# Kernel optimization log

Hardware: AMD Instinct MI355X
Metric: run time of the kernel (lower is better)

## Reference

```python
import jax, jax.numpy as jnp
import numpy as np

INPUT_SIZE = 1024
HIDDEN_SIZE = 1024
BATCH = 8192


def setup_inputs() -> dict:
    key = jax.random.key(0)
    ks = jax.random.split(key, 10)
    s_in = 1.0 / np.sqrt(INPUT_SIZE)
    s_h = 1.0 / np.sqrt(HIDDEN_SIZE)
    return {
        "input": jax.random.normal(ks[0], (BATCH, INPUT_SIZE), jnp.float32),
        "hx": jax.random.normal(ks[1], (BATCH, HIDDEN_SIZE), jnp.float32),
        # weights stored [in, out] (transpose of torch Linear)
        "W_ih": jax.random.uniform(ks[2], (INPUT_SIZE, 2 * HIDDEN_SIZE), jnp.float32, -s_in, s_in),
        "b_ih": jax.random.uniform(ks[3], (2 * HIDDEN_SIZE,), jnp.float32, -s_in, s_in),
        "W_hh": jax.random.uniform(ks[4], (HIDDEN_SIZE, 2 * HIDDEN_SIZE), jnp.float32, -s_h, s_h),
        "b_hh": jax.random.uniform(ks[5], (2 * HIDDEN_SIZE,), jnp.float32, -s_h, s_h),
        "W_c": jax.random.uniform(ks[6], (INPUT_SIZE, HIDDEN_SIZE), jnp.float32, -s_in, s_in),
        "b_c": jax.random.uniform(ks[7], (HIDDEN_SIZE,), jnp.float32, -s_in, s_in),
        "W_hc": jax.random.uniform(ks[8], (HIDDEN_SIZE, HIDDEN_SIZE), jnp.float32, -s_h, s_h),
        "b_hc": jax.random.uniform(ks[9], (HIDDEN_SIZE,), jnp.float32, -s_h, s_h),
    }


def reference(input, hx, W_ih, b_ih, W_hh, b_hh, W_c, b_c, W_hc, b_hc):
    H = hx.shape[1]
    gates = jax.nn.sigmoid(input @ W_ih + b_ih + hx @ W_hh + b_hh)  # [B, 2H]
    z_t, r_t = gates[:, :H], gates[:, H:]
    candidate = jnp.tanh(input @ W_c + b_c + r_t * (hx @ W_hc + b_hc))
    return (1.0 - z_t) * hx + z_t * candidate
```

## Files before the change

kernel.cpp:

```cpp
#include <hip/hip_runtime.h>
#include <hip/hip_bf16.h>
#include <cmath>


typedef __attribute__((ext_vector_type(8))) short bf16x8;
typedef __attribute__((ext_vector_type(4))) float f32x4;
typedef unsigned int u32;

typedef const __attribute__((address_space(1))) u32 gu32;
typedef __attribute__((address_space(3))) u32 su32;

__device__ __forceinline__ unsigned short f2bf(float f) {
  union { float f; u32 u; } v; v.f = f;
  u32 u = v.u;
  u += 0x7FFFu + ((u >> 16) & 1u);
  return (unsigned short)(u >> 16);
}
__device__ __forceinline__ void gload16(void* ldsp, const void* gp) {
  __builtin_amdgcn_global_load_lds((gu32*)gp, (su32*)ldsp, 16, 0, 0);
}
__device__ __forceinline__ float sigmf(float x) { return 1.0f / (1.0f + __expf(-x)); }

__global__ __launch_bounds__(256) void cvt_all(
    const float* __restrict__ In, const float* __restrict__ Hx,
    const float* __restrict__ Wih, const float* __restrict__ Whh,
    const float* __restrict__ Wc,  const float* __restrict__ Whc,
    unsigned short* __restrict__ wsIn, unsigned short* __restrict__ wsHx,
    unsigned short* __restrict__ wsWih, unsigned short* __restrict__ wsWhh,
    unsigned short* __restrict__ wsWc,  unsigned short* __restrict__ wsWhc)
{
  int bid = blockIdx.x;
  if (bid < 8192) {
    int gid = bid * 256 + threadIdx.x;
    const float* src; unsigned short* dst; int idx;
    if (gid < (1 << 20)) { src = In; dst = wsIn; idx = gid; }
    else                 { src = Hx; dst = wsHx; idx = gid - (1 << 20); }
    int m = idx >> 7, t = idx & 127;
    const float4* s = (const float4*)(src + (size_t)m * 1024 + t * 8);
    float4 a = s[0], b = s[1];
    int row = m & 127;
    size_t tile = (size_t)(m >> 7) * 32 + (t >> 2);
    int sw = (t & 3) ^ ((row >> 1) & 3);
    bf16x8 v;
    v[0] = (short)f2bf(a.x); v[1] = (short)f2bf(a.y); v[2] = (short)f2bf(a.z); v[3] = (short)f2bf(a.w);
    v[4] = (short)f2bf(b.x); v[5] = (short)f2bf(b.y); v[6] = (short)f2bf(b.z); v[7] = (short)f2bf(b.w);
    *(bf16x8*)(dst + tile * 4096 + row * 32 + sw * 8) = v;
  } else {
    int wb = bid - 8192;
    const float* W; unsigned short* dst; int NW; int local;
    if (wb < 1024)      { W = Wih; dst = wsWih; NW = 2048; local = wb; }
    else if (wb < 2048) { W = Whh; dst = wsWhh; NW = 2048; local = wb - 1024; }
    else if (wb < 2560) { W = Wc;  dst = wsWc;  NW = 1024; local = wb - 2048; }
    else                { W = Whc; dst = wsWhc; NW = 1024; local = wb - 2560; }
    int nb = local >> 5, kb = local & 31;
    int n  = nb * 64 + (threadIdx.x & 63);
    int k0 = kb * 32 + (threadIdx.x >> 6) * 8;
    bf16x8 v;
    #pragma unroll
    for (int b = 0; b < 8; ++b) v[b] = (short)f2bf(W[(size_t)(k0 + b) * NW + n]);
    int row = n & 63;
    size_t tile = (size_t)(n >> 6) * 32 + (k0 >> 5);
    int sw = ((k0 >> 3) & 3) ^ ((row >> 1) & 3);
    *(bf16x8*)(dst + tile * 2048 + row * 32 + sw * 8) = v;
  }
}

__global__ __launch_bounds__(256, 2) void gru_gemm(
    const unsigned short* __restrict__ wsIn, const unsigned short* __restrict__ wsHx,
    const unsigned short* __restrict__ wsWih, const unsigned short* __restrict__ wsWhh,
    const unsigned short* __restrict__ wsWc, const unsigned short* __restrict__ wsWhc,
    const float* __restrict__ Hx,
    const float* __restrict__ bih, const float* __restrict__ bhh,
    const float* __restrict__ bc, const float* __restrict__ bhc,
    float* __restrict__ out)
{
  __shared__ unsigned short lds[40960];
  const int tid  = threadIdx.x;
  const int lane = tid & 63;
  const int wave = tid >> 6;
  const int wm = wave >> 1, wn = wave & 1;
  const int bid = blockIdx.x;
  const int swz = (bid & 7) * 128 + (bid >> 3);
  const int j = swz & 15;
  const int i = swz >> 4;

  const unsigned short* srcB[10];
  int strd[10];
  #pragma unroll
  for (int c0 = 0; c0 < 10; ++c0) {
    int c = wave * 10 + c0;
    const unsigned short* p; int st;
    if (c < 8)       { p = wsIn + (size_t)i * 131072 + c * 512;        st = 4096; }
    else if (c < 16) { p = wsHx + (size_t)i * 131072 + (c - 8) * 512;  st = 4096; }
    else {
      int t = (c - 16) >> 2, cc = (c - 16) & 3;
      const unsigned short* base; int nb;
      if (t == 0)      { base = wsWih; nb = j; }
      else if (t == 1) { base = wsWih; nb = j + 16; }
      else if (t == 2) { base = wsWhh; nb = j; }
      else if (t == 3) { base = wsWhh; nb = j + 16; }
      else if (t == 4) { base = wsWc;  nb = j; }
      else             { base = wsWhc; nb = j; }
      p = base + (size_t)nb * 65536 + cc * 512;
      st = 2048;
    }
    srcB[c0] = p + lane * 8;
    strd[c0] = st;
  }
  const int stageOff = (wave * 10) * 512;

  f32x4 accZ[4][2], accR[4][2], accC[4][2], accH[4][2];
  #pragma unroll
  for (int a = 0; a < 4; ++a)
    #pragma unroll
    for (int b = 0; b < 2; ++b) {
      accZ[a][b] = (f32x4)(0.0f); accR[a][b] = (f32x4)(0.0f);
      accC[a][b] = (f32x4)(0.0f); accH[a][b] = (f32x4)(0.0f);
    }

  const int r15 = lane & 15;
  const int q   = lane >> 4;

  int aOff[4], wOff[2];
  #pragma unroll
  for (int mr = 0; mr < 4; ++mr) {
    int row = wm * 64 + mr * 16 + r15;
    aOff[mr] = row * 32 + ((q ^ ((row >> 1) & 3)) << 3);
  }
  #pragma unroll
  for (int nr = 0; nr < 2; ++nr) {
    int row = wn * 32 + nr * 16 + r15;
    wOff[nr] = row * 32 + ((q ^ ((row >> 1) & 3)) << 3);
  }

  auto stage = [&](int bufBase, int s) {
    #pragma unroll
    for (int c0 = 0; c0 < 10; ++c0)
      gload16((void*)&lds[bufBase + stageOff + c0 * 512],
              (const void*)(srcB[c0] + (size_t)s * strd[c0]));
  };

  auto compute = [&](const unsigned short* __restrict__ L) {
    bf16x8 aIn[4], aHx[4];
    #pragma unroll
    for (int mr = 0; mr < 4; ++mr) {
      aIn[mr] = *(const bf16x8*)&L[aOff[mr]];
      aHx[mr] = *(const bf16x8*)&L[4096 + aOff[mr]];
    }
    bf16x8 wf[6][2];
    #pragma unroll
    for (int t = 0; t < 6; ++t)
      #pragma unroll
      for (int nr = 0; nr < 2; ++nr)
        wf[t][nr] = *(const bf16x8*)&L[8192 + t * 2048 + wOff[nr]];

    #pragma unroll
    for (int mr = 0; mr < 4; ++mr)
      #pragma unroll
      for (int nr = 0; nr < 2; ++nr) {
        accZ[mr][nr] = __builtin_amdgcn_mfma_f32_16x16x32_bf16(aIn[mr], wf[0][nr], accZ[mr][nr], 0, 0, 0);
        accZ[mr][nr] = __builtin_amdgcn_mfma_f32_16x16x32_bf16(aHx[mr], wf[2][nr], accZ[mr][nr], 0, 0, 0);
        accR[mr][nr] = __builtin_amdgcn_mfma_f32_16x16x32_bf16(aIn[mr], wf[1][nr], accR[mr][nr], 0, 0, 0);
        accR[mr][nr] = __builtin_amdgcn_mfma_f32_16x16x32_bf16(aHx[mr], wf[3][nr], accR[mr][nr], 0, 0, 0);
        accC[mr][nr] = __builtin_amdgcn_mfma_f32_16x16x32_bf16(aIn[mr], wf[4][nr], accC[mr][nr], 0, 0, 0);
        accH[mr][nr] = __builtin_amdgcn_mfma_f32_16x16x32_bf16(aHx[mr], wf[5][nr], accH[mr][nr], 0, 0, 0);
      }
  };

  stage(0, 0);
  __syncthreads();

  #pragma unroll 1
  for (int it = 0; it < 16; ++it) {
    const int s = it * 2;
    stage(20480, s + 1);
    compute(&lds[0]);
    __syncthreads();
    if (it < 15) stage(0, s + 2);
    compute(&lds[20480]);
    __syncthreads();
  }

  const int n0 = j * 64 + wn * 32;
  const int m0 = i * 128 + wm * 64;
  #pragma unroll
  for (int nr = 0; nr < 2; ++nr) {
    int n = n0 + nr * 16 + r15;
    float bz  = bih[n] + bhh[n];
    float br  = bih[1024 + n] + bhh[1024 + n];
    float bcv = bc[n], bhcv = bhc[n];
    #pragma unroll
    for (int mr = 0; mr < 4; ++mr) {
      #pragma unroll
      for (int v = 0; v < 4; ++v) {
        int m = m0 + mr * 16 + q * 4 + v;
        float z  = sigmf(accZ[mr][nr][v] + bz);
        float rr = sigmf(accR[mr][nr][v] + br);
        float cd = tanhf(accC[mr][nr][v] + bcv + rr * (accH[mr][nr][v] + bhcv));
        float h  = Hx[(size_t)m * 1024 + n];
        out[(size_t)m * 1024 + n] = (1.0f - z) * h + z * cd;
      }
    }
  }
}

__global__ __launch_bounds__(256) void gru_fallback(
    const float* __restrict__ In, const float* __restrict__ Hx,
    const float* __restrict__ Wih, const float* __restrict__ bih,
    const float* __restrict__ Whh, const float* __restrict__ bhh,
    const float* __restrict__ Wc, const float* __restrict__ bc,
    const float* __restrict__ Whc, const float* __restrict__ bhc,
    float* __restrict__ out)
{
  __shared__ float sIn[64][17], sHx[64][17];
  __shared__ float sW[6][16][68];
  const int tid = threadIdx.x;
  const int j = blockIdx.x & 15, i = blockIdx.x >> 4;
  const int tx = tid & 15, ty = tid >> 4;
  float accZ[4][4] = {}, accR[4][4] = {}, accC[4][4] = {}, accH[4][4] = {};
  const int ms = tid >> 2, kq = (tid & 3) * 4;
  const int wk = tid >> 4, wn4 = (tid & 15) * 4;
  for (int k0 = 0; k0 < 1024; k0 += 16) {
    __syncthreads();
    {
      float4 a = *(const float4*)&In[(size_t)(i * 64 + ms) * 1024 + k0 + kq];
      sIn[ms][kq] = a.x; sIn[ms][kq + 1] = a.y; sIn[ms][kq + 2] = a.z; sIn[ms][kq + 3] = a.w;
      float4 b = *(const float4*)&Hx[(size_t)(i * 64 + ms) * 1024 + k0 + kq];
      sHx[ms][kq] = b.x; sHx[ms][kq + 1] = b.y; sHx[ms][kq + 2] = b.z; sHx[ms][kq + 3] = b.w;
    }
    {
      float4 w0 = *(const float4*)&Wih[(size_t)(k0 + wk) * 2048 + j * 64 + wn4];
      float4 w1 = *(const float4*)&Wih[(size_t)(k0 + wk) * 2048 + 1024 + j * 64 + wn4];
      float4 w2 = *(const float4*)&Whh[(size_t)(k0 + wk) * 2048 + j * 64 + wn4];
      float4 w3 = *(const float4*)&Whh[(size_t)(k0 + wk) * 2048 + 1024 + j * 64 + wn4];
      float4 w4 = *(const float4*)&Wc[(size_t)(k0 + wk) * 1024 + j * 64 + wn4];
      float4 w5 = *(const float4*)&Whc[(size_t)(k0 + wk) * 1024 + j * 64 + wn4];
      sW[0][wk][wn4] = w0.x; sW[0][wk][wn4+1] = w0.y; sW[0][wk][wn4+2] = w0.z; sW[0][wk][wn4+3] = w0.w;
      sW[1][wk][wn4] = w1.x; sW[1][wk][wn4+1] = w1.y; sW[1][wk][wn4+2] = w1.z; sW[1][wk][wn4+3] = w1.w;
      sW[2][wk][wn4] = w2.x; sW[2][wk][wn4+1] = w2.y; sW[2][wk][wn4+2] = w2.z; sW[2][wk][wn4+3] = w2.w;
      sW[3][wk][wn4] = w3.x; sW[3][wk][wn4+1] = w3.y; sW[3][wk][wn4+2] = w3.z; sW[3][wk][wn4+3] = w3.w;
      sW[4][wk][wn4] = w4.x; sW[4][wk][wn4+1] = w4.y; sW[4][wk][wn4+2] = w4.z; sW[4][wk][wn4+3] = w4.w;
      sW[5][wk][wn4] = w5.x; sW[5][wk][wn4+1] = w5.y; sW[5][wk][wn4+2] = w5.z; sW[5][wk][wn4+3] = w5.w;
    }
    __syncthreads();
    for (int kk = 0; kk < 16; ++kk) {
      float aI[4], aH[4];
      #pragma unroll
      for (int im = 0; im < 4; ++im) { aI[im] = sIn[ty * 4 + im][kk]; aH[im] = sHx[ty * 4 + im][kk]; }
      #pragma unroll
      for (int jn = 0; jn < 4; ++jn) {
        float w0 = sW[0][kk][tx * 4 + jn], w1 = sW[1][kk][tx * 4 + jn], w2 = sW[2][kk][tx * 4 + jn];
        float w3 = sW[3][kk][tx * 4 + jn], w4 = sW[4][kk][tx * 4 + jn], w5 = sW[5][kk][tx * 4 + jn];
        #pragma unroll
        for (int im = 0; im < 4; ++im) {
          accZ[im][jn] += aI[im] * w0 + aH[im] * w2;
          accR[im][jn] += aI[im] * w1 + aH[im] * w3;
          accC[im][jn] += aI[im] * w4;
          accH[im][jn] += aH[im] * w5;
        }
      }
    }
  }
  #pragma unroll
  for (int jn = 0; jn < 4; ++jn) {
    int n = j * 64 + tx * 4 + jn;
    float bz  = bih[n] + bhh[n];
    float br  = bih[1024 + n] + bhh[1024 + n];
    float bcv = bc[n], bhcv = bhc[n];
    #pragma unroll
    for (int im = 0; im < 4; ++im) {
      int m = i * 64 + ty * 4 + im;
      float z  = sigmf(accZ[im][jn] + bz);
      float rr = sigmf(accR[im][jn] + br);
      float cd = tanhf(accC[im][jn] + bcv + rr * (accH[im][jn] + bhcv));
      float h  = Hx[(size_t)m * 1024 + n];
      out[(size_t)m * 1024 + n] = (1.0f - z) * h + z * cd;
    }
  }
}

extern "C" void kernel_launch(void* const* d_in, const int* in_sizes, int n_in,
                              void* d_out, int out_size, void* d_ws, size_t ws_size,
                              hipStream_t stream) {
  const float* In  = (const float*)d_in[0];
  const float* Hx  = (const float*)d_in[1];
  const float* Wih = (const float*)d_in[2];
  const float* bih = (const float*)d_in[3];
  const float* Whh = (const float*)d_in[4];
  const float* bhh = (const float*)d_in[5];
  const float* Wc  = (const float*)d_in[6];
  const float* bc  = (const float*)d_in[7];
  const float* Whc = (const float*)d_in[8];
  const float* bhc = (const float*)d_in[9];
  float* out = (float*)d_out;

  const size_t WS_NEED = 46137344ull;
  if (ws_size >= WS_NEED) {
    unsigned short* ws    = (unsigned short*)d_ws;
    unsigned short* wsIn  = ws;
    unsigned short* wsHx  = ws + 8388608;
    unsigned short* wsWih = ws + 16777216;
    unsigned short* wsWhh = ws + 18874368;
    unsigned short* wsWc  = ws + 20971520;
    unsigned short* wsWhc = ws + 22020096;
    cvt_all<<<11264, 256, 0, stream>>>(In, Hx, Wih, Whh, Wc, Whc,
                                       wsIn, wsHx, wsWih, wsWhh, wsWc, wsWhc);
    gru_gemm<<<1024, 256, 0, stream>>>(wsIn, wsHx, wsWih, wsWhh, wsWc, wsWhc,
                                       Hx, bih, bhh, bc, bhc, out);
  } else {
    gru_fallback<<<2048, 256, 0, stream>>>(In, Hx, Wih, bih, Whh, bhh, Wc, bc, Whc, bhc, out);
  }
}
```

Before: 139.3 us.

## Load weight fragments directly from global memory, stage only activations in LDS

The GEMM kernel now stages only the input and hidden-state tiles through LDS. Each wave reads its weight fragments straight from the pre-swizzled workspace in global memory into registers, which shrinks shared memory from 80KB to 32KB per block. Block indexing also changes from the grouped swizzle to i = bid & 63, j = bid >> 6, so consecutive blocks share the same weight tile. The aim is to cut LDS traffic and footprint and raise occupancy. The cost is uncoalesced-ish global/L2 weight reads on the critical path, since each wave loads its own weights with no cross-wave reuse through LDS.

```diff
diff --git a/kernel.cpp b/kernel.cpp
--- a/kernel.cpp
+++ b/kernel.cpp
@@ -66,48 +66,48 @@
 }
 
 __global__ __launch_bounds__(256, 2) void gru_gemm(
-    const unsigned short* __restrict__ wsIn, const unsigned short* __restrict__ wsHx,
-    const unsigned short* __restrict__ wsWih, const unsigned short* __restrict__ wsWhh,
-    const unsigned short* __restrict__ wsWc, const unsigned short* __restrict__ wsWhc,
+    const unsigned short* __restrict__ ws,
     const float* __restrict__ Hx,
     const float* __restrict__ bih, const float* __restrict__ bhh,
     const float* __restrict__ bc, const float* __restrict__ bhc,
     float* __restrict__ out)
 {
-  __shared__ unsigned short lds[40960];
+  __shared__ unsigned short lds[16384];
   const int tid  = threadIdx.x;
   const int lane = tid & 63;
   const int wave = tid >> 6;
   const int wm = wave >> 1, wn = wave & 1;
   const int bid = blockIdx.x;
-  const int swz = (bid & 7) * 128 + (bid >> 3);
-  const int j = swz & 15;
-  const int i = swz >> 4;
-
-  const unsigned short* srcB[10];
-  int strd[10];
-  #pragma unroll
-  for (int c0 = 0; c0 < 10; ++c0) {
-    int c = wave * 10 + c0;
-    const unsigned short* p; int st;
-    if (c < 8)       { p = wsIn + (size_t)i * 131072 + c * 512;        st = 4096; }
-    else if (c < 16) { p = wsHx + (size_t)i * 131072 + (c - 8) * 512;  st = 4096; }
-    else {
-      int t = (c - 16) >> 2, cc = (c - 16) & 3;
-      const unsigned short* base; int nb;
-      if (t == 0)      { base = wsWih; nb = j; }
-      else if (t == 1) { base = wsWih; nb = j + 16; }
-      else if (t == 2) { base = wsWhh; nb = j; }
-      else if (t == 3) { base = wsWhh; nb = j + 16; }
-      else if (t == 4) { base = wsWc;  nb = j; }
-      else             { base = wsWhc; nb = j; }
-      p = base + (size_t)nb * 65536 + cc * 512;
-      st = 2048;
-    }
-    srcB[c0] = p + lane * 8;
-    strd[c0] = st;
-  }
-  const int stageOff = (wave * 10) * 512;
+  const int i = bid & 63;
+  const int j = bid >> 6;
+  const int r15 = lane & 15;
+  const int q   = lane >> 4;
+
+  u32 wb[6];
+  wb[0] = 16777216u + (u32)j * 65536u;
+  wb[1] = 16777216u + (u32)(j + 16) * 65536u;
+  wb[2] = 18874368u + (u32)j * 65536u;
+  wb[3] = 18874368u + (u32)(j + 16) * 65536u;
+  wb[4] = 20971520u + (u32)j * 65536u;
+  wb[5] = 22020096u + (u32)j * 65536u;
+  const int rw = wn * 32 + r15;
+  const u32 vo = (u32)(rw * 32 + ((q ^ ((rw >> 1) & 3)) << 3));
+
+  const unsigned short* srcA[4];
+  #pragma unroll
+  for (int c0 = 0; c0 < 4; ++c0) {
+    int c = wave * 4 + c0;
+    srcA[c0] = (c < 8 ? ws + (size_t)i * 131072 + c * 512
+                      : ws + 8388608 + (size_t)i * 131072 + (c - 8) * 512) + lane * 8;
+  }
+  const int dstA = wave * 4 * 512;
+
+  int aOff[4];
+  #pragma unroll
+  for (int mr = 0; mr < 4; ++mr) {
+    int row = wm * 64 + mr * 16 + r15;
+    aOff[mr] = row * 32 + ((q ^ ((row >> 1) & 3)) << 3);
+  }
 
   f32x4 accZ[4][2], accR[4][2], accC[4][2], accH[4][2];
   #pragma unroll
@@ -118,42 +118,27 @@
       accC[a][b] = (f32x4)(0.0f); accH[a][b] = (f32x4)(0.0f);
     }
 
-  const int r15 = lane & 15;
-  const int q   = lane >> 4;
-
-  int aOff[4], wOff[2];
-  #pragma unroll
-  for (int mr = 0; mr < 4; ++mr) {
-    int row = wm * 64 + mr * 16 + r15;
-    aOff[mr] = row * 32 + ((q ^ ((row >> 1) & 3)) << 3);
-  }
-  #pragma unroll
-  for (int nr = 0; nr < 2; ++nr) {
-    int row = wn * 32 + nr * 16 + r15;
-    wOff[nr] = row * 32 + ((q ^ ((row >> 1) & 3)) << 3);
-  }
-
   auto stage = [&](int bufBase, int s) {
     #pragma unroll
-    for (int c0 = 0; c0 < 10; ++c0)
-      gload16((void*)&lds[bufBase + stageOff + c0 * 512],
-              (const void*)(srcB[c0] + (size_t)s * strd[c0]));
+    for (int c0 = 0; c0 < 4; ++c0)
+      gload16((void*)&lds[bufBase + dstA + c0 * 512],
+              (const void*)(srcA[c0] + (size_t)s * 4096));
   };
 
-  auto compute = [&](const unsigned short* __restrict__ L) {
+  auto step = [&](int B, int t, int OB, int sNext, bool doStage) {
+    bf16x8 wf[6][2];
+    #pragma unroll
+    for (int m = 0; m < 6; ++m) {
+      wf[m][0] = *(const bf16x8*)(ws + wb[m] + (u32)t * 2048u + vo);
+      wf[m][1] = *(const bf16x8*)(ws + wb[m] + (u32)t * 2048u + vo + 512u);
+    }
+    if (doStage) stage(OB, sNext);
     bf16x8 aIn[4], aHx[4];
     #pragma unroll
     for (int mr = 0; mr < 4; ++mr) {
-      aIn[mr] = *(const bf16x8*)&L[aOff[mr]];
-      aHx[mr] = *(const bf16x8*)&L[4096 + aOff[mr]];
-    }
-    bf16x8 wf[6][2];
-    #pragma unroll
-    for (int t = 0; t < 6; ++t)
-      #pragma unroll
-      for (int nr = 0; nr < 2; ++nr)
-        wf[t][nr] = *(const bf16x8*)&L[8192 + t * 2048 + wOff[nr]];
-
+      aIn[mr] = *(const bf16x8*)&lds[B + aOff[mr]];
+      aHx[mr] = *(const bf16x8*)&lds[B + 4096 + aOff[mr]];
+    }
     #pragma unroll
     for (int mr = 0; mr < 4; ++mr)
       #pragma unroll
@@ -165,6 +150,7 @@
         accC[mr][nr] = __builtin_amdgcn_mfma_f32_16x16x32_bf16(aIn[mr], wf[4][nr], accC[mr][nr], 0, 0, 0);
         accH[mr][nr] = __builtin_amdgcn_mfma_f32_16x16x32_bf16(aHx[mr], wf[5][nr], accH[mr][nr], 0, 0, 0);
       }
+    __syncthreads();
   };
 
   stage(0, 0);
@@ -173,12 +159,8 @@
   #pragma unroll 1
   for (int it = 0; it < 16; ++it) {
     const int s = it * 2;
-    stage(20480, s + 1);
-    compute(&lds[0]);
-    __syncthreads();
-    if (it < 15) stage(0, s + 2);
-    compute(&lds[20480]);
-    __syncthreads();
+    step(0,    s,     8192, s + 1, true);
+    step(8192, s + 1, 0,    s + 2, it < 15);
   }
 
   const int n0 = j * 64 + wn * 32;
@@ -305,8 +287,7 @@
     unsigned short* wsWhc = ws + 22020096;
     cvt_all<<<11264, 256, 0, stream>>>(In, Hx, Wih, Whh, Wc, Whc,
                                        wsIn, wsHx, wsWih, wsWhh, wsWc, wsWhc);
-    gru_gemm<<<1024, 256, 0, stream>>>(wsIn, wsHx, wsWih, wsWhh, wsWc, wsWhc,
-                                       Hx, bih, bhh, bc, bhc, out);
+    gru_gemm<<<1024, 256, 0, stream>>>(ws, Hx, bih, bhh, bc, bhc, out);
   } else {
     gru_fallback<<<2048, 256, 0, stream>>>(In, Hx, Wih, bih, Whh, bhh, Wc, bc, Whc, bhc, out);
   }
```

Measured after the change: 147.6 us. 1.06x slower.

## Switch GRU GEMM to 32x32x16 MFMA with fragment-native bf16 packing

Applied to the files above, without the earlier changes.

Replaces the 16x16x32 MFMA tiles with 32x32x16 bf16 MFMA and rewrites the conversion kernel so inputs and weights are stored in a layout where each lane's 16-byte fragment lies contiguously in LDS. This removes the XOR swizzle and per-row offset arithmetic, and halves the number of MFMA instructions issued per K step. The block-index swizzle used for L2 locality is also dropped in favour of plain row-major block ordering. Risks include LDS bank conflicts on the new contiguous layout, worse L2 reuse without the swizzle, and an epilogue whose column-wise stores may coalesce less well.

```diff
diff --git a/kernel.cpp b/kernel.cpp
--- a/kernel.cpp
+++ b/kernel.cpp
@@ -3,8 +3,8 @@
 #include <cmath>
 
 
-typedef __attribute__((ext_vector_type(8))) short bf16x8;
-typedef __attribute__((ext_vector_type(4))) float f32x4;
+typedef __attribute__((ext_vector_type(8)))  short bf16x8;
+typedef __attribute__((ext_vector_type(16))) float f32x16;
 typedef unsigned int u32;
 
 typedef const __attribute__((address_space(1))) u32 gu32;
@@ -38,13 +38,12 @@
     int m = idx >> 7, t = idx & 127;
     const float4* s = (const float4*)(src + (size_t)m * 1024 + t * 8);
     float4 a = s[0], b = s[1];
-    int row = m & 127;
-    size_t tile = (size_t)(m >> 7) * 32 + (t >> 2);
-    int sw = (t & 3) ^ ((row >> 1) & 3);
+    int mt = m >> 5, row = m & 31;
+    int kt = t >> 2, ksub = (t >> 1) & 1, half = t & 1;
     bf16x8 v;
     v[0] = (short)f2bf(a.x); v[1] = (short)f2bf(a.y); v[2] = (short)f2bf(a.z); v[3] = (short)f2bf(a.w);
     v[4] = (short)f2bf(b.x); v[5] = (short)f2bf(b.y); v[6] = (short)f2bf(b.z); v[7] = (short)f2bf(b.w);
-    *(bf16x8*)(dst + tile * 4096 + row * 32 + sw * 8) = v;
+    *(bf16x8*)(dst + ((size_t)(mt * 32 + kt) * 2 + ksub) * 512 + half * 256 + row * 8) = v;
   } else {
     int wb = bid - 8192;
     const float* W; unsigned short* dst; int NW; int local;
@@ -53,15 +52,15 @@
     else if (wb < 2560) { W = Wc;  dst = wsWc;  NW = 1024; local = wb - 2048; }
     else                { W = Whc; dst = wsWhc; NW = 1024; local = wb - 2560; }
     int nb = local >> 5, kb = local & 31;
-    int n  = nb * 64 + (threadIdx.x & 63);
-    int k0 = kb * 32 + (threadIdx.x >> 6) * 8;
+    int tid = threadIdx.x;
+    int n  = nb * 64 + (tid & 63);
+    int k0 = kb * 32 + (tid >> 6) * 8;
     bf16x8 v;
     #pragma unroll
     for (int b = 0; b < 8; ++b) v[b] = (short)f2bf(W[(size_t)(k0 + b) * NW + n]);
-    int row = n & 63;
-    size_t tile = (size_t)(n >> 6) * 32 + (k0 >> 5);
-    int sw = ((k0 >> 3) & 3) ^ ((row >> 1) & 3);
-    *(bf16x8*)(dst + tile * 2048 + row * 32 + sw * 8) = v;
+    int ct = n >> 5, row = n & 31;
+    int ksub = (tid >> 7), half = (tid >> 6) & 1;
+    *(bf16x8*)(dst + ((size_t)(ct * 32 + kb) * 2 + ksub) * 512 + half * 256 + row * 8) = v;
   }
 }
 
@@ -80,90 +79,76 @@
   const int wave = tid >> 6;
   const int wm = wave >> 1, wn = wave & 1;
   const int bid = blockIdx.x;
-  const int swz = (bid & 7) * 128 + (bid >> 3);
-  const int j = swz & 15;
-  const int i = swz >> 4;
+  const int j = bid & 15;
+  const int i = bid >> 4;
+  const int lo = lane * 8;
 
   const unsigned short* srcB[10];
-  int strd[10];
   #pragma unroll
   for (int c0 = 0; c0 < 10; ++c0) {
     int c = wave * 10 + c0;
-    const unsigned short* p; int st;
-    if (c < 8)       { p = wsIn + (size_t)i * 131072 + c * 512;        st = 4096; }
-    else if (c < 16) { p = wsHx + (size_t)i * 131072 + (c - 8) * 512;  st = 4096; }
-    else {
-      int t = (c - 16) >> 2, cc = (c - 16) & 3;
-      const unsigned short* base; int nb;
-      if (t == 0)      { base = wsWih; nb = j; }
-      else if (t == 1) { base = wsWih; nb = j + 16; }
-      else if (t == 2) { base = wsWhh; nb = j; }
-      else if (t == 3) { base = wsWhh; nb = j + 16; }
-      else if (t == 4) { base = wsWc;  nb = j; }
-      else             { base = wsWhc; nb = j; }
-      p = base + (size_t)nb * 65536 + cc * 512;
-      st = 2048;
-    }
-    srcB[c0] = p + lane * 8;
-    strd[c0] = st;
+    const unsigned short* p;
+    if (c < 8) {
+      p = wsIn + ((size_t)(i * 4 + (c >> 1)) * 64 + (c & 1)) * 512;
+    } else if (c < 16) {
+      int cc = c - 8;
+      p = wsHx + ((size_t)(i * 4 + (cc >> 1)) * 64 + (cc & 1)) * 512;
+    } else {
+      int cc = c - 16, mat = cc >> 2, q = cc & 3, cs = q >> 1, s = q & 1;
+      const unsigned short* base; int ct;
+      if (mat == 0)      { base = wsWih; ct = 2 * j + cs; }
+      else if (mat == 1) { base = wsWhh; ct = 2 * j + cs; }
+      else if (mat == 2) { base = wsWih; ct = 32 + 2 * j + cs; }
+      else if (mat == 3) { base = wsWhh; ct = 32 + 2 * j + cs; }
+      else if (mat == 4) { base = wsWc;  ct = 2 * j + cs; }
+      else               { base = wsWhc; ct = 2 * j + cs; }
+      p = base + ((size_t)ct * 64 + s) * 512;
+    }
+    srcB[c0] = p + lo;
   }
   const int stageOff = (wave * 10) * 512;
 
-  f32x4 accZ[4][2], accR[4][2], accC[4][2], accH[4][2];
-  #pragma unroll
-  for (int a = 0; a < 4; ++a)
-    #pragma unroll
-    for (int b = 0; b < 2; ++b) {
-      accZ[a][b] = (f32x4)(0.0f); accR[a][b] = (f32x4)(0.0f);
-      accC[a][b] = (f32x4)(0.0f); accH[a][b] = (f32x4)(0.0f);
-    }
-
-  const int r15 = lane & 15;
-  const int q   = lane >> 4;
-
-  int aOff[4], wOff[2];
-  #pragma unroll
-  for (int mr = 0; mr < 4; ++mr) {
-    int row = wm * 64 + mr * 16 + r15;
-    aOff[mr] = row * 32 + ((q ^ ((row >> 1) & 3)) << 3);
-  }
-  #pragma unroll
-  for (int nr = 0; nr < 2; ++nr) {
-    int row = wn * 32 + nr * 16 + r15;
-    wOff[nr] = row * 32 + ((q ^ ((row >> 1) & 3)) << 3);
-  }
-
-  auto stage = [&](int bufBase, int s) {
+  f32x16 accZ[2], accR[2], accC[2], accH[2];
+  #pragma unroll
+  for (int a = 0; a < 2; ++a) {
+    accZ[a] = (f32x16)(0.0f); accR[a] = (f32x16)(0.0f);
+    accC[a] = (f32x16)(0.0f); accH[a] = (f32x16)(0.0f);
+  }
+
+  auto stage = [&](int bufBase, int kt) {
     #pragma unroll
     for (int c0 = 0; c0 < 10; ++c0)
       gload16((void*)&lds[bufBase + stageOff + c0 * 512],
-              (const void*)(srcB[c0] + (size_t)s * strd[c0]));
+              (const void*)(srcB[c0] + (size_t)kt * 1024));
   };
 
+  #define MFMA32(a, b, c) __builtin_amdgcn_mfma_f32_32x32x16_bf16(a, b, c, 0, 0, 0)
+
   auto compute = [&](const unsigned short* __restrict__ L) {
-    bf16x8 aIn[4], aHx[4];
-    #pragma unroll
-    for (int mr = 0; mr < 4; ++mr) {
-      aIn[mr] = *(const bf16x8*)&L[aOff[mr]];
-      aHx[mr] = *(const bf16x8*)&L[4096 + aOff[mr]];
-    }
-    bf16x8 wf[6][2];
-    #pragma unroll
-    for (int t = 0; t < 6; ++t)
-      #pragma unroll
-      for (int nr = 0; nr < 2; ++nr)
-        wf[t][nr] = *(const bf16x8*)&L[8192 + t * 2048 + wOff[nr]];
-
-    #pragma unroll
-    for (int mr = 0; mr < 4; ++mr)
-      #pragma unroll
-      for (int nr = 0; nr < 2; ++nr) {
-        accZ[mr][nr] = __builtin_amdgcn_mfma_f32_16x16x32_bf16(aIn[mr], wf[0][nr], accZ[mr][nr], 0, 0, 0);
-        accZ[mr][nr] = __builtin_amdgcn_mfma_f32_16x16x32_bf16(aHx[mr], wf[2][nr], accZ[mr][nr], 0, 0, 0);
-        accR[mr][nr] = __builtin_amdgcn_mfma_f32_16x16x32_bf16(aIn[mr], wf[1][nr], accR[mr][nr], 0, 0, 0);
-        accR[mr][nr] = __builtin_amdgcn_mfma_f32_16x16x32_bf16(aHx[mr], wf[3][nr], accR[mr][nr], 0, 0, 0);
-        accC[mr][nr] = __builtin_amdgcn_mfma_f32_16x16x32_bf16(aIn[mr], wf[4][nr], accC[mr][nr], 0, 0, 0);
-        accH[mr][nr] = __builtin_amdgcn_mfma_f32_16x16x32_bf16(aHx[mr], wf[5][nr], accH[mr][nr], 0, 0, 0);
+    bf16x8 aIn[2][2], aHx[2][2], w[6][2];
+    #pragma unroll
+    for (int mtl = 0; mtl < 2; ++mtl)
+      #pragma unroll
+      for (int s = 0; s < 2; ++s) {
+        aIn[mtl][s] = *(const bf16x8*)&L[((wm * 2 + mtl) * 2 + s) * 512 + lo];
+        aHx[mtl][s] = *(const bf16x8*)&L[(8 + (wm * 2 + mtl) * 2 + s) * 512 + lo];
+      }
+    #pragma unroll
+    for (int mat = 0; mat < 6; ++mat)
+      #pragma unroll
+      for (int s = 0; s < 2; ++s)
+        w[mat][s] = *(const bf16x8*)&L[(16 + mat * 4 + wn * 2 + s) * 512 + lo];
+
+    #pragma unroll
+    for (int s = 0; s < 2; ++s)
+      #pragma unroll
+      for (int mtl = 0; mtl < 2; ++mtl) {
+        accZ[mtl] = MFMA32(aIn[mtl][s], w[0][s], accZ[mtl]);
+        accZ[mtl] = MFMA32(aHx[mtl][s], w[1][s], accZ[mtl]);
+        accR[mtl] = MFMA32(aIn[mtl][s], w[2][s], accR[mtl]);
+        accR[mtl] = MFMA32(aHx[mtl][s], w[3][s], accR[mtl]);
+        accC[mtl] = MFMA32(aIn[mtl][s], w[4][s], accC[mtl]);
+        accH[mtl] = MFMA32(aHx[mtl][s], w[5][s], accH[mtl]);
       }
   };
 
@@ -181,27 +166,25 @@
     __syncthreads();
   }
 
-  const int n0 = j * 64 + wn * 32;
-  const int m0 = i * 128 + wm * 64;
-  #pragma unroll
-  for (int nr = 0; nr < 2; ++nr) {
-    int n = n0 + nr * 16 + r15;
-    float bz  = bih[n] + bhh[n];
-    float br  = bih[1024 + n] + bhh[1024 + n];
-    float bcv = bc[n], bhcv = bhc[n];
-    #pragma unroll
-    for (int mr = 0; mr < 4; ++mr) {
-      #pragma unroll
-      for (int v = 0; v < 4; ++v) {
-        int m = m0 + mr * 16 + q * 4 + v;
-        float z  = sigmf(accZ[mr][nr][v] + bz);
-        float rr = sigmf(accR[mr][nr][v] + br);
-        float cd = tanhf(accC[mr][nr][v] + bcv + rr * (accH[mr][nr][v] + bhcv));
-        float h  = Hx[(size_t)m * 1024 + n];
-        out[(size_t)m * 1024 + n] = (1.0f - z) * h + z * cd;
-      }
-    }
-  }
+  const int n = j * 64 + wn * 32 + (lane & 31);
+  const float bz  = bih[n] + bhh[n];
+  const float br  = bih[1024 + n] + bhh[1024 + n];
+  const float bcv = bc[n], bhcv = bhc[n];
+  const int rowb = 4 * (lane >> 5);
+  #pragma unroll
+  for (int mtl = 0; mtl < 2; ++mtl) {
+    #pragma unroll
+    for (int r = 0; r < 16; ++r) {
+      int row = (r & 3) + 8 * (r >> 2) + rowb;
+      int m = i * 128 + wm * 64 + mtl * 32 + row;
+      float z  = sigmf(accZ[mtl][r] + bz);
+      float rr = sigmf(accR[mtl][r] + br);
+      float cd = tanhf(accC[mtl][r] + bcv + rr * (accH[mtl][r] + bhcv));
+      float h  = Hx[(size_t)m * 1024 + n];
+      out[(size_t)m * 1024 + n] = (1.0f - z) * h + z * cd;
+    }
+  }
+  #undef MFMA32
 }
 
 __global__ __launch_bounds__(256) void gru_fallback(
```

After: 151.4 us. 1.09x slower.
